# Performance work log

Hardware: AMD Instinct MI355X
Metric: run time of the kernel (lower is better)

## Reference

```python
import jax, jax.numpy as jnp
import numpy as np
import jax.scipy.linalg as jsl

N_SAMPLES = 100000
N_COMPONENTS = 64
N_FEATURES = 32
LOW, HIGH = -0.1, 0.1


def setup_inputs() -> dict:
    key = jax.random.key(0)
    k_x, k_mu = jax.random.split(key)
    X = jax.random.normal(k_x, (N_SAMPLES, N_FEATURES), dtype=jnp.float32)
    means = jax.random.uniform(k_mu, (N_COMPONENTS, N_FEATURES),
                               minval=LOW, maxval=HIGH, dtype=jnp.float32)
    # torch init: stack of tril(eye(D)) == identity for each component
    eye = jnp.eye(N_FEATURES, dtype=jnp.float32)
    scale_tril = jnp.tile(eye[None, :, :], (N_COMPONENTS, 1, 1))
    log_weights = jnp.zeros((N_COMPONENTS,), dtype=jnp.float32)
    return {"X": X, "means": means, "scale_tril": scale_tril,
            "log_weights": log_weights}


def reference(X, means, scale_tril, log_weights):
    N, D = X.shape
    LOG_2PI = jnp.log(jnp.asarray(2.0 * np.pi, dtype=X.dtype))

    def comp_log_prob(mu, L):
        # MVN log-prob via triangular whitening (matches torch MVN(scale_tril=L))
        diff = (X - mu).T                     # [D, N]
        z = jsl.solve_triangular(L, diff, lower=True)  # [D, N]
        maha = jnp.sum(z * z, axis=0)          # [N]
        half_logdet = jnp.sum(jnp.log(jnp.diagonal(L)))
        return -0.5 * (D * LOG_2PI + maha) - half_logdet  # [N]

    logp = jax.vmap(comp_log_prob)(means, scale_tril)  # [K, N]

    # E-step: responsibilities (raw exp, as in the original; no logsumexp)
    weights = jax.nn.softmax(log_weights)              # [K]
    unnorm = weights[:, None] * jnp.exp(logp)          # [K, N]
    resp = unnorm / jnp.sum(unnorm, axis=0, keepdims=True)  # [K, N]

    # M-step: note torch's F.log_softmax(log_weights[k], dim=-1) on a 0-d
    # tensor is identically 0 (softmax of a single element), so it is omitted.
    log_likelihood = jnp.sum(resp * logp, axis=0)      # [N]
    return -jnp.mean(log_likelihood)
```

## Files before the change

kernel.cpp:

```cpp
#include <hip/hip_runtime.h>
#include <math.h>

#define NS 100000
#define NC 64
#define ND 32
#define NK 576
#define NBLK ((NS + 127) / 128)
#define QBYTES (NC * NK * 2)
#define LOG2PI 1.8378770664093453f

typedef __attribute__((ext_vector_type(8))) __bf16 bf16x8;
typedef __attribute__((ext_vector_type(8))) float  floatx8;
typedef __attribute__((ext_vector_type(4))) float  floatx4;



template<int I, int L>
__device__ __forceinline__ void fsub_inner(const float* Ls, const float (&a)[ND], float& s) {
    if constexpr (L < I) {
        s = fmaf(-Ls[I * ND + L], a[L], s);
        fsub_inner<I, L + 1>(Ls, a, s);
    }
}

template<int I>
__device__ __forceinline__ void fsub(const float* Ls, float (&a)[ND], int j) {
    if constexpr (I < ND) {
        float s = (I == j) ? 1.0f : 0.0f;
        fsub_inner<I, 0>(Ls, a, s);
        float v = s / Ls[I * ND + I];
        a[I] = (I < j) ? 0.0f : v;
        fsub<I + 1>(Ls, a, j);
    }
}

__global__ void gmm_setup(const float* __restrict__ means,
                          const float* __restrict__ scale_tril,
                          const float* __restrict__ log_weights,
                          __bf16* __restrict__ Qf,
                          float* __restrict__ lw,
                          float* __restrict__ kc) {
    int k = blockIdx.x;
    int tid = threadIdx.x;
    __shared__ float Ls[ND * ND];
    __shared__ float Ac[ND][ND + 1];
    __shared__ float P[ND][ND + 1];
    __shared__ float bb[ND];
    __shared__ float mu_s[ND];

    for (int idx = tid; idx < ND * ND; idx += 64)
        Ls[idx] = scale_tril[(size_t)k * ND * ND + idx];
    if (tid < ND) mu_s[tid] = means[k * ND + tid];
    __syncthreads();

    if (tid < ND) {
        int j = tid;
        float a[ND];
        fsub<0>(Ls, a, j);
#pragma unroll
        for (int i = 0; i < ND; ++i) Ac[j][i] = a[i];
    }
    __syncthreads();

    {
        int i = tid & 31, h = tid >> 5;
        for (int j = 16 * h; j < 16 * h + 16; ++j) {
            float s = 0.0f;
#pragma unroll
            for (int l = 0; l < ND; ++l) s += Ac[i][l] * Ac[j][l];
            P[i][j] = s;
        }
    }
    __syncthreads();
    if (tid < ND) {
        float s = 0.0f;
        for (int j = 0; j < ND; ++j) s += P[tid][j] * mu_s[j];
        bb[tid] = s;
    }
    __syncthreads();

    int mt = k >> 4, colk = k & 15;
    for (int kf = tid; kf < NK; kf += 64) {
        int t = kf >> 5, u = kf & 31;
        int quad = u >> 3, jj = u & 7;
        float val;
        if (t == 0) val = -0.5f * P[u][u];
        else if (t < 16) val = -P[u][(u + t) & 31];
        else if (t == 16) val = (u < 16) ? -P[u][u + 16] : bb[u - 16];
        else val = (u < 16) ? bb[16 + u] : 0.0f;
        Qf[(size_t)(((mt * 18 + t) * 64 + quad * 16 + colk) * 8 + jj)] = (__bf16)val;
    }

    if (tid == 0) {
        float cc = 0.0f, hld = 0.0f;
        for (int i = 0; i < ND; ++i) { cc += mu_s[i] * bb[i]; hld += logf(Ls[i * ND + i]); }
        kc[k] = -0.5f * cc + (-0.5f * (float)ND * LOG2PI - hld);
    }
    if (k == 0) {
        float mx = log_weights[0];
        for (int t = 1; t < NC; ++t) mx = fmaxf(mx, log_weights[t]);
        float se = 0.0f;
        for (int t = 0; t < NC; ++t) se += __expf(log_weights[t] - mx);
        lw[tid] = log_weights[tid] - mx - logf(se);
    }
}


template<int G>
__device__ __forceinline__ void fill_x(const float4* p, float (&xr)[ND], int quad) {
    if constexpr (G < 8) {
        float4 v = p[(G + 2 * quad) & 7];
        xr[4 * G + 0] = v.x; xr[4 * G + 1] = v.y;
        xr[4 * G + 2] = v.z; xr[4 * G + 3] = v.w;
        fill_x<G + 1>(p, xr, quad);
    }
}

template<int T, int JJ>
__device__ __forceinline__ void feat(const float (&xr0)[ND], const float (&xr1)[ND],
                                     int quad, floatx8& f0, floatx8& f1) {
    if constexpr (JJ < 8) {
        float a0, a1, b0, b1;
        if constexpr (T < 16) {
            a0 = xr0[JJ]; b0 = xr0[(JJ + T) & 31];
            a1 = xr1[JJ]; b1 = xr1[(JJ + T) & 31];
        } else if constexpr (T == 16) {
            a0 = (quad < 2) ? xr0[JJ] : 1.0f;  b0 = xr0[(JJ + 16) & 31];
            a1 = (quad < 2) ? xr1[JJ] : 1.0f;  b1 = xr1[(JJ + 16) & 31];
        } else {
            a0 = (quad < 2) ? xr0[(JJ + 16) & 31] : 0.0f; b0 = 1.0f;
            a1 = (quad < 2) ? xr1[(JJ + 16) & 31] : 0.0f; b1 = 1.0f;
        }
        f0[JJ] = a0 * b0;
        f1[JJ] = a1 * b1;
        feat<T, JJ + 1>(xr0, xr1, quad, f0, f1);
    }
}

template<int T, int MT>
__device__ __forceinline__ void mfma_step(const unsigned char* qlane, bf16x8 b0, bf16x8 b1,
                                          floatx4 (&A0)[4], floatx4 (&A1)[4]) {
    if constexpr (MT < 4) {
        bf16x8 af = *(const bf16x8*)(qlane + (MT * 18 + T) * 1024);
        A0[MT] = __builtin_amdgcn_mfma_f32_16x16x32_bf16(af, b0, A0[MT], 0, 0, 0);
        A1[MT] = __builtin_amdgcn_mfma_f32_16x16x32_bf16(af, b1, A1[MT], 0, 0, 0);
        mfma_step<T, MT + 1>(qlane, b0, b1, A0, A1);
    }
}

template<int T>
__device__ __forceinline__ void kloop(const unsigned char* qlane,
                                      const float (&xr0)[ND], const float (&xr1)[ND],
                                      int quad, floatx4 (&A0)[4], floatx4 (&A1)[4]) {
    if constexpr (T < 18) {
        floatx8 f0, f1;
        feat<T, 0>(xr0, xr1, quad, f0, f1);
        bf16x8 b0 = __builtin_convertvector(f0, bf16x8);
        bf16x8 b1 = __builtin_convertvector(f1, bf16x8);
        mfma_step<T, 0>(qlane, b0, b1, A0, A1);
        kloop<T + 1>(qlane, xr0, xr1, quad, A0, A1);
    }
}

template<int MT, int R>
__device__ __forceinline__ void epi_r(const floatx4 (&A0)[4], const floatx4 (&A1)[4],
                                      floatx4 lwv, floatx4 kcv,
                                      float& s0, float& w0, float& s1, float& w1) {
    if constexpr (R < 4) {
        float lp0 = A0[MT][R] + kcv[R];
        float e0 = __expf(lp0 + lwv[R]);
        s0 += e0; w0 = fmaf(e0, lp0, w0);
        float lp1 = A1[MT][R] + kcv[R];
        float e1 = __expf(lp1 + lwv[R]);
        s1 += e1; w1 = fmaf(e1, lp1, w1);
        epi_r<MT, R + 1>(A0, A1, lwv, kcv, s0, w0, s1, w1);
    }
}

template<int MT>
__device__ __forceinline__ void epi(const float* lw_s, const float* kc_s, int quad,
                                    const floatx4 (&A0)[4], const floatx4 (&A1)[4],
                                    float& s0, float& w0, float& s1, float& w1) {
    if constexpr (MT < 4) {
        floatx4 lwv = *(const floatx4*)&lw_s[MT * 16 + quad * 4];
        floatx4 kcv = *(const floatx4*)&kc_s[MT * 16 + quad * 4];
        epi_r<MT, 0>(A0, A1, lwv, kcv, s0, w0, s1, w1);
        epi<MT + 1>(lw_s, kc_s, quad, A0, A1, s0, w0, s1, w1);
    }
}

__launch_bounds__(256, 2)
__global__ void gmm_main(const float* __restrict__ X,
                         const __bf16* __restrict__ Qf,
                         const float* __restrict__ lw,
                         const float* __restrict__ kc,
                         float* __restrict__ pb) {
    __shared__ __align__(16) unsigned char qlds[QBYTES];
    __shared__ float lw_s[NC];
    __shared__ float kc_s[NC];
    __shared__ float partial[4];
    int tid = threadIdx.x;
    if (tid < NC) { lw_s[tid] = lw[tid]; kc_s[tid] = kc[tid]; }
    {
        const float4* gsrc = (const float4*)Qf;
        float4* ldst = (float4*)qlds;
#pragma unroll
        for (int i = 0; i < QBYTES / 16 / 256; ++i)
            ldst[i * 256 + tid] = gsrc[i * 256 + tid];
    }
    __syncthreads();

    const int lane = tid & 63;
    const int wave = tid >> 6;
    const int quad = lane >> 4;

    int n0 = blockIdx.x * 128 + wave * 32 + (lane & 15);
    int n1 = n0 + 16;
    int n0c = n0 < NS ? n0 : NS - 1;
    int n1c = n1 < NS ? n1 : NS - 1;

    float xr0[ND], xr1[ND];
    fill_x<0>((const float4*)(X + (size_t)n0c * ND), xr0, quad);
    fill_x<0>((const float4*)(X + (size_t)n1c * ND), xr1, quad);

    floatx4 A0[4], A1[4];
#pragma unroll
    for (int mt = 0; mt < 4; ++mt) {
        A0[mt] = (floatx4){0.f, 0.f, 0.f, 0.f};
        A1[mt] = (floatx4){0.f, 0.f, 0.f, 0.f};
    }

    kloop<0>(qlds + lane * 16, xr0, xr1, quad, A0, A1);

    float s0 = 0.f, w0 = 0.f, s1 = 0.f, w1 = 0.f;
    epi<0>(lw_s, kc_s, quad, A0, A1, s0, w0, s1, w1);

    s0 += __shfl_xor(s0, 16); s0 += __shfl_xor(s0, 32);
    w0 += __shfl_xor(w0, 16); w0 += __shfl_xor(w0, 32);
    s1 += __shfl_xor(s1, 16); s1 += __shfl_xor(s1, 32);
    w1 += __shfl_xor(w1, 16); w1 += __shfl_xor(w1, 32);

    float ll = 0.0f;
    ll += (n0 < NS) ? (w0 / s0) : 0.0f;
    ll += (n1 < NS) ? (w1 / s1) : 0.0f;

#pragma unroll
    for (int off = 1; off < 64; off <<= 1) ll += __shfl_xor(ll, off);
    if (lane == 0) partial[wave] = ll * 0.25f;
    __syncthreads();

    if (tid == 0)
        pb[blockIdx.x] = partial[0] + partial[1] + partial[2] + partial[3];
}

__global__ void gmm_reduce(const float* __restrict__ pb, float* __restrict__ out) {
    int tid = threadIdx.x;
    float s = 0.0f;
    for (int i = tid; i < NBLK; i += 256) s += pb[i];
#pragma unroll
    for (int off = 32; off > 0; off >>= 1) s += __shfl_down(s, off);
    __shared__ float wsum[4];
    if ((tid & 63) == 0) wsum[tid >> 6] = s;
    __syncthreads();
    if (tid == 0)
        out[0] = -(wsum[0] + wsum[1] + wsum[2] + wsum[3]) / (float)NS;
}

extern "C" void kernel_launch(void* const* d_in, const int* in_sizes, int n_in,
                              void* d_out, int out_size, void* d_ws, size_t ws_size,
                              hipStream_t stream) {
    const float* X           = (const float*)d_in[0];
    const float* means       = (const float*)d_in[1];
    const float* scale_tril  = (const float*)d_in[2];
    const float* log_weights = (const float*)d_in[3];

    char* ws = (char*)d_ws;
    __bf16* Qf = (__bf16*)ws;
    float*  lw = (float*)(ws + 73728);
    float*  kc = (float*)(ws + 73984);
    float*  pb = (float*)(ws + 74240);

    gmm_setup<<<NC, 64, 0, stream>>>(means, scale_tril, log_weights, Qf, lw, kc);
    gmm_main<<<NBLK, 256, 0, stream>>>(X, Qf, lw, kc, pb);
    gmm_reduce<<<1, 256, 0, stream>>>(pb, (float*)d_out);
}
```

Baseline: 97.79 us.

## Use persistent grid with last-block reduction and drop separate reduce kernel

```diff
diff --git a/kernel.cpp b/kernel.cpp
--- a/kernel.cpp
+++ b/kernel.cpp
@@ -5,7 +5,8 @@
 #define NC 64
 #define ND 32
 #define NK 576
-#define NBLK ((NS + 127) / 128)
+#define NCHUNK ((NS + 127) / 128)
+#define GRID 512
 #define QBYTES (NC * NK * 2)
 #define LOG2PI 1.8378770664093453f
 
@@ -39,7 +40,8 @@
                           const float* __restrict__ log_weights,
                           __bf16* __restrict__ Qf,
                           float* __restrict__ lw,
-                          float* __restrict__ kc) {
+                          float* __restrict__ kc,
+                          unsigned int* __restrict__ counter) {
     int k = blockIdx.x;
     int tid = threadIdx.x;
     __shared__ float Ls[ND * ND];
@@ -102,6 +104,7 @@
         float se = 0.0f;
         for (int t = 0; t < NC; ++t) se += __expf(log_weights[t] - mx);
         lw[tid] = log_weights[tid] - mx - logf(se);
+        if (tid == 0) counter[0] = 0u;
     }
 }
 
@@ -194,11 +197,14 @@
                          const __bf16* __restrict__ Qf,
                          const float* __restrict__ lw,
                          const float* __restrict__ kc,
-                         float* __restrict__ pb) {
+                         float* __restrict__ pb,
+                         unsigned int* __restrict__ counter,
+                         float* __restrict__ out) {
     __shared__ __align__(16) unsigned char qlds[QBYTES];
     __shared__ float lw_s[NC];
     __shared__ float kc_s[NC];
     __shared__ float partial[4];
+    __shared__ int is_last;
     int tid = threadIdx.x;
     if (tid < NC) { lw_s[tid] = lw[tid]; kc_s[tid] = kc[tid]; }
     {
@@ -214,56 +220,64 @@
     const int wave = tid >> 6;
     const int quad = lane >> 4;
 
-    int n0 = blockIdx.x * 128 + wave * 32 + (lane & 15);
-    int n1 = n0 + 16;
-    int n0c = n0 < NS ? n0 : NS - 1;
-    int n1c = n1 < NS ? n1 : NS - 1;
-
-    float xr0[ND], xr1[ND];
-    fill_x<0>((const float4*)(X + (size_t)n0c * ND), xr0, quad);
-    fill_x<0>((const float4*)(X + (size_t)n1c * ND), xr1, quad);
-
-    floatx4 A0[4], A1[4];
-#pragma unroll
-    for (int mt = 0; mt < 4; ++mt) {
-        A0[mt] = (floatx4){0.f, 0.f, 0.f, 0.f};
-        A1[mt] = (floatx4){0.f, 0.f, 0.f, 0.f};
-    }
-
-    kloop<0>(qlds + lane * 16, xr0, xr1, quad, A0, A1);
-
-    float s0 = 0.f, w0 = 0.f, s1 = 0.f, w1 = 0.f;
-    epi<0>(lw_s, kc_s, quad, A0, A1, s0, w0, s1, w1);
-
-    s0 += __shfl_xor(s0, 16); s0 += __shfl_xor(s0, 32);
-    w0 += __shfl_xor(w0, 16); w0 += __shfl_xor(w0, 32);
-    s1 += __shfl_xor(s1, 16); s1 += __shfl_xor(s1, 32);
-    w1 += __shfl_xor(w1, 16); w1 += __shfl_xor(w1, 32);
-
     float ll = 0.0f;
-    ll += (n0 < NS) ? (w0 / s0) : 0.0f;
-    ll += (n1 < NS) ? (w1 / s1) : 0.0f;
+
+    for (int chunk = blockIdx.x; chunk < NCHUNK; chunk += GRID) {
+        int n0 = chunk * 128 + wave * 32 + (lane & 15);
+        int n1 = n0 + 16;
+        int n0c = n0 < NS ? n0 : NS - 1;
+        int n1c = n1 < NS ? n1 : NS - 1;
+
+        float xr0[ND], xr1[ND];
+        fill_x<0>((const float4*)(X + (size_t)n0c * ND), xr0, quad);
+        fill_x<0>((const float4*)(X + (size_t)n1c * ND), xr1, quad);
+
+        floatx4 A0[4], A1[4];
+#pragma unroll
+        for (int mt = 0; mt < 4; ++mt) {
+            A0[mt] = (floatx4){0.f, 0.f, 0.f, 0.f};
+            A1[mt] = (floatx4){0.f, 0.f, 0.f, 0.f};
+        }
+
+        kloop<0>(qlds + lane * 16, xr0, xr1, quad, A0, A1);
+
+        float s0 = 0.f, w0 = 0.f, s1 = 0.f, w1 = 0.f;
+        epi<0>(lw_s, kc_s, quad, A0, A1, s0, w0, s1, w1);
+
+        s0 += __shfl_xor(s0, 16); s0 += __shfl_xor(s0, 32);
+        w0 += __shfl_xor(w0, 16); w0 += __shfl_xor(w0, 32);
+        s1 += __shfl_xor(s1, 16); s1 += __shfl_xor(s1, 32);
+        w1 += __shfl_xor(w1, 16); w1 += __shfl_xor(w1, 32);
+
+        ll += (n0 < NS) ? (w0 / s0) : 0.0f;
+        ll += (n1 < NS) ? (w1 / s1) : 0.0f;
+    }
 
 #pragma unroll
     for (int off = 1; off < 64; off <<= 1) ll += __shfl_xor(ll, off);
     if (lane == 0) partial[wave] = ll * 0.25f;
     __syncthreads();
 
-    if (tid == 0)
+    if (tid == 0) {
         pb[blockIdx.x] = partial[0] + partial[1] + partial[2] + partial[3];
-}
-
-__global__ void gmm_reduce(const float* __restrict__ pb, float* __restrict__ out) {
-    int tid = threadIdx.x;
-    float s = 0.0f;
-    for (int i = tid; i < NBLK; i += 256) s += pb[i];
-#pragma unroll
-    for (int off = 32; off > 0; off >>= 1) s += __shfl_down(s, off);
-    __shared__ float wsum[4];
-    if ((tid & 63) == 0) wsum[tid >> 6] = s;
-    __syncthreads();
-    if (tid == 0)
-        out[0] = -(wsum[0] + wsum[1] + wsum[2] + wsum[3]) / (float)NS;
+        __threadfence();
+        unsigned int tk = atomicAdd(counter, 1u);
+        is_last = (tk == GRID - 1) ? 1 : 0;
+    }
+    __syncthreads();
+
+    if (is_last) {
+        __threadfence();
+        float s = (tid < GRID) ? pb[tid] : 0.0f;
+        s += (tid + 256 < GRID) ? pb[tid + 256] : 0.0f;
+#pragma unroll
+        for (int off = 32; off > 0; off >>= 1) s += __shfl_down(s, off);
+        __shared__ float wsum[4];
+        if ((tid & 63) == 0) wsum[tid >> 6] = s;
+        __syncthreads();
+        if (tid == 0)
+            out[0] = -(wsum[0] + wsum[1] + wsum[2] + wsum[3]) / (float)NS;
+    }
 }
 
 extern "C" void kernel_launch(void* const* d_in, const int* in_sizes, int n_in,
@@ -275,12 +289,13 @@
     const float* log_weights = (const float*)d_in[3];
 
     char* ws = (char*)d_ws;
-    __bf16* Qf = (__bf16*)ws;
-    float*  lw = (float*)(ws + 73728);
-    float*  kc = (float*)(ws + 73984);
-    float*  pb = (float*)(ws + 74240);
-
-    gmm_setup<<<NC, 64, 0, stream>>>(means, scale_tril, log_weights, Qf, lw, kc);
-    gmm_main<<<NBLK, 256, 0, stream>>>(X, Qf, lw, kc, pb);
-    gmm_reduce<<<1, 256, 0, stream>>>(pb, (float*)d_out);
-}
+    __bf16*       Qf      = (__bf16*)ws;
+    float*        lw      = (float*)(ws + 73728);
+    float*        kc      = (float*)(ws + 73984);
+    float*        pb      = (float*)(ws + 74240);
+    unsigned int* counter = (unsigned int*)(ws + 76544);
+
+    gmm_setup<<<NC, 64, 0, stream>>>(means, scale_tril, log_weights,
+                                     Qf, lw, kc, counter);
+    gmm_main<<<GRID, 256, 0, stream>>>(X, Qf, lw, kc, pb, counter, (float*)d_out);
+}
```

New measurement: 149.5 us. 1.53x slower.

## Batch eight components per setup block with vectorized LDS and wave reductions

Applied to the files above, without the earlier changes.

```diff
diff --git a/kernel.cpp b/kernel.cpp
--- a/kernel.cpp
+++ b/kernel.cpp
@@ -7,6 +7,7 @@
 #define NK 576
 #define NBLK ((NS + 127) / 128)
 #define QBYTES (NC * NK * 2)
+#define NCPB 8
 #define LOG2PI 1.8378770664093453f
 
 typedef __attribute__((ext_vector_type(8))) __bf16 bf16x8;
@@ -15,93 +16,161 @@
 
 
 
+template<int I, int Q>
+__device__ __forceinline__ void load_row(const floatx4* ls4, floatx4 (&rb)[8]) {
+    if constexpr (Q <= I / 4) {
+        rb[Q] = ls4[I * 8 + Q];
+        load_row<I, Q + 1>(ls4, rb);
+    }
+}
+
 template<int I, int L>
-__device__ __forceinline__ void fsub_inner(const float* Ls, const float (&a)[ND], float& s) {
+__device__ __forceinline__ void fchain(const floatx4 (&rb)[8], const float (&a)[ND], float& s) {
     if constexpr (L < I) {
-        s = fmaf(-Ls[I * ND + L], a[L], s);
-        fsub_inner<I, L + 1>(Ls, a, s);
+        s = fmaf(-rb[L / 4][L % 4], a[L], s);
+        fchain<I, L + 1>(rb, a, s);
     }
 }
 
 template<int I>
-__device__ __forceinline__ void fsub(const float* Ls, float (&a)[ND], int j) {
+__device__ __forceinline__ void fsub2(const floatx4* ls4, float (&a)[ND], int j) {
     if constexpr (I < ND) {
+        floatx4 rb[8];
+        load_row<I, 0>(ls4, rb);
         float s = (I == j) ? 1.0f : 0.0f;
-        fsub_inner<I, 0>(Ls, a, s);
-        float v = s / Ls[I * ND + I];
+        fchain<I, 0>(rb, a, s);
+        float v = s / rb[I / 4][I % 4];
         a[I] = (I < j) ? 0.0f : v;
-        fsub<I + 1>(Ls, a, j);
-    }
-}
-
+        fsub2<I + 1>(ls4, a, j);
+    }
+}
+
+template<int Q>
+__device__ __forceinline__ void store_ac(float* acrow, const float (&a)[ND]) {
+    if constexpr (Q < 8) {
+        floatx4 t;
+        t[0] = a[4 * Q + 0]; t[1] = a[4 * Q + 1];
+        t[2] = a[4 * Q + 2]; t[3] = a[4 * Q + 3];
+        *(floatx4*)(acrow + 4 * Q) = t;
+        store_ac<Q + 1>(acrow, a);
+    }
+}
+
+template<int JJ>
+__device__ __forceinline__ void qpack(bf16x8& v, const float* Pc, const float* bbc,
+                                      int t, int quad) {
+    if constexpr (JJ < 8) {
+        int u = quad * 8 + JJ;
+        float val;
+        if (t == 0)       val = -0.5f * Pc[u * 32 + u];
+        else if (t < 16)  val = -Pc[u * 32 + ((u + t) & 31)];
+        else if (t == 16) val = (u < 16) ? -Pc[u * 32 + u + 16] : bbc[u - 16];
+        else              val = (u < 16) ? bbc[16 + u] : 0.0f;
+        v[JJ] = (__bf16)val;
+        qpack<JJ + 1>(v, Pc, bbc, t, quad);
+    }
+}
+
+__launch_bounds__(512)
 __global__ void gmm_setup(const float* __restrict__ means,
                           const float* __restrict__ scale_tril,
                           const float* __restrict__ log_weights,
                           __bf16* __restrict__ Qf,
                           float* __restrict__ lw,
                           float* __restrict__ kc) {
-    int k = blockIdx.x;
-    int tid = threadIdx.x;
-    __shared__ float Ls[ND * ND];
-    __shared__ float Ac[ND][ND + 1];
-    __shared__ float P[ND][ND + 1];
-    __shared__ float bb[ND];
-    __shared__ float mu_s[ND];
-
-    for (int idx = tid; idx < ND * ND; idx += 64)
-        Ls[idx] = scale_tril[(size_t)k * ND * ND + idx];
-    if (tid < ND) mu_s[tid] = means[k * ND + tid];
-    __syncthreads();
-
-    if (tid < ND) {
-        int j = tid;
+    __shared__ __align__(16) floatx4 LsP4[NCPB * 256];
+    __shared__ __align__(16) float Ac[NCPB][32][36];
+    __shared__ float mu_s[NCPB][32];
+    __shared__ float bb_s[NCPB][32];
+
+    const int tid  = threadIdx.x;
+    const int b    = blockIdx.x;
+    const int w    = tid >> 6;
+    const int lane = tid & 63;
+
+    {
+        const floatx4* g4 = (const floatx4*)scale_tril + (size_t)b * 2048;
+#pragma unroll
+        for (int q = 0; q < 4; ++q)
+            LsP4[q * 512 + tid] = g4[q * 512 + tid];
+        if (tid < NCPB * 32)
+            mu_s[tid >> 5][tid & 31] = means[(size_t)(b * NCPB + (tid >> 5)) * ND + (tid & 31)];
+    }
+    __syncthreads();
+
+    const floatx4* ls4 = LsP4 + w * 256;
+    if (lane < ND) {
         float a[ND];
-        fsub<0>(Ls, a, j);
-#pragma unroll
-        for (int i = 0; i < ND; ++i) Ac[j][i] = a[i];
-    }
+        fsub2<0>(ls4, a, lane);
+        store_ac<0>(&Ac[w][lane][0], a);
+    }
+    float hv = (lane < ND) ? logf(((const float*)LsP4)[w * 1024 + lane * 33]) : 0.0f;
+#pragma unroll
+    for (int off = 1; off < 64; off <<= 1) hv += __shfl_xor(hv, off);
+    float hld = hv;
     __syncthreads();
 
     {
-        int i = tid & 31, h = tid >> 5;
-        for (int j = 16 * h; j < 16 * h + 16; ++j) {
+        int c = tid >> 6, half = (tid >> 5) & 1, i = tid & 31;
+        const floatx4* rI4 = (const floatx4*)&Ac[c][i][0];
+        float* Pc = (float*)LsP4 + c * 1024;
+        for (int j16 = 0; j16 < 16; ++j16) {
+            int j = half * 16 + j16;
+            const floatx4* rJ4 = (const floatx4*)&Ac[c][j][0];
             float s = 0.0f;
 #pragma unroll
-            for (int l = 0; l < ND; ++l) s += Ac[i][l] * Ac[j][l];
-            P[i][j] = s;
+            for (int q = 0; q < 8; ++q) {
+                floatx4 x = rI4[q], y = rJ4[q];
+                s = fmaf(x[0], y[0], s); s = fmaf(x[1], y[1], s);
+                s = fmaf(x[2], y[2], s); s = fmaf(x[3], y[3], s);
+            }
+            Pc[i * 32 + j] = s;
         }
     }
     __syncthreads();
-    if (tid < ND) {
-        float s = 0.0f;
-        for (int j = 0; j < ND; ++j) s += P[tid][j] * mu_s[j];
-        bb[tid] = s;
-    }
-    __syncthreads();
-
-    int mt = k >> 4, colk = k & 15;
-    for (int kf = tid; kf < NK; kf += 64) {
-        int t = kf >> 5, u = kf & 31;
-        int quad = u >> 3, jj = u & 7;
-        float val;
-        if (t == 0) val = -0.5f * P[u][u];
-        else if (t < 16) val = -P[u][(u + t) & 31];
-        else if (t == 16) val = (u < 16) ? -P[u][u + 16] : bb[u - 16];
-        else val = (u < 16) ? bb[16 + u] : 0.0f;
-        Qf[(size_t)(((mt * 18 + t) * 64 + quad * 16 + colk) * 8 + jj)] = (__bf16)val;
-    }
-
-    if (tid == 0) {
-        float cc = 0.0f, hld = 0.0f;
-        for (int i = 0; i < ND; ++i) { cc += mu_s[i] * bb[i]; hld += logf(Ls[i * ND + i]); }
-        kc[k] = -0.5f * cc + (-0.5f * (float)ND * LOG2PI - hld);
-    }
-    if (k == 0) {
-        float mx = log_weights[0];
-        for (int t = 1; t < NC; ++t) mx = fmaxf(mx, log_weights[t]);
-        float se = 0.0f;
-        for (int t = 0; t < NC; ++t) se += __expf(log_weights[t] - mx);
-        lw[tid] = log_weights[tid] - mx - logf(se);
+
+    const float* Pw = (const float*)LsP4 + w * 1024;
+    float bbv = 0.0f;
+    if (lane < ND) {
+        for (int j = 0; j < ND; ++j) bbv = fmaf(Pw[lane * 32 + j], mu_s[w][j], bbv);
+        bb_s[w][lane] = bbv;
+    }
+    float ccv = (lane < ND) ? mu_s[w][lane] * bbv : 0.0f;
+#pragma unroll
+    for (int off = 1; off < 64; off <<= 1) ccv += __shfl_xor(ccv, off);
+    int comp = b * NCPB + w;
+    if (lane == 0)
+        kc[comp] = -0.5f * ccv - 16.0f * LOG2PI - hld;
+
+    if (b == 0 && w == 0) {
+        float x = log_weights[lane];
+        float mx = x;
+#pragma unroll
+        for (int off = 1; off < 64; off <<= 1) mx = fmaxf(mx, __shfl_xor(mx, off));
+        float e = __expf(x - mx);
+#pragma unroll
+        for (int off = 1; off < 64; off <<= 1) e += __shfl_xor(e, off);
+        lw[lane] = x - mx - logf(e);
+    }
+
+    {
+        int mt = comp >> 4, colk = comp & 15;
+        const float* bbc = &bb_s[w][0];
+        bf16x8* qdst = (bf16x8*)Qf;
+        int cl = lane;
+        {
+            int t = cl >> 2, quad = cl & 3;
+            bf16x8 v;
+            qpack<0>(v, Pw, bbc, t, quad);
+            qdst[(size_t)(mt * 18 + t) * 64 + quad * 16 + colk] = v;
+        }
+        if (lane < 8) {
+            int cl2 = 64 + lane;
+            int t = cl2 >> 2, quad = cl2 & 3;
+            bf16x8 v;
+            qpack<0>(v, Pw, bbc, t, quad);
+            qdst[(size_t)(mt * 18 + t) * 64 + quad * 16 + colk] = v;
+        }
     }
 }
 
@@ -280,7 +349,7 @@
     float*  kc = (float*)(ws + 73984);
     float*  pb = (float*)(ws + 74240);
 
-    gmm_setup<<<NC, 64, 0, stream>>>(means, scale_tril, log_weights, Qf, lw, kc);
+    gmm_setup<<<NC / NCPB, 512, 0, stream>>>(means, scale_tril, log_weights, Qf, lw, kc);
     gmm_main<<<NBLK, 256, 0, stream>>>(X, Qf, lw, kc, pb);
     gmm_reduce<<<1, 256, 0, stream>>>(pb, (float*)d_out);
 }
```

Measured after the change: 95.75 us. 2.1% less time.
